# Optimization experiments

Measured on AMD Instinct MI355X. Metric: run time of the kernel, lower is better.

Reference implementation:

```python
import jax, jax.numpy as jnp
import numpy as np

B, C, H, W, N, K = 1, 64, 256, 1216, 40000, 9
EPS = 1e-5  # torch BatchNorm2d default eps


def setup_inputs() -> dict:
    key = jax.random.key(0)
    ks = jax.random.split(key, 10)
    feature_tensor = jax.random.normal(ks[0], (B, C, H, W), jnp.float32)
    nn_diff_pts_3d = jax.random.normal(ks[1], (B, N, K, 3), jnp.float32)
    # (x, y) pixel coords; 0..255 valid for both H=256 rows and W=1216 cols
    pixel_idxs = jax.random.randint(ks[2], (B, N, 2), 0, 256, dtype=jnp.int64)
    nn_pixel_idxs = jax.random.randint(ks[3], (B, N, K, 2), 0, 256, dtype=jnp.int64)
    W1 = jax.random.normal(ks[4], (3, C // 2), jnp.float32) * (1.0 / np.sqrt(3.0))
    b1 = jnp.zeros((C // 2,), jnp.float32)
    W2 = jax.random.normal(ks[5], (C // 2, C), jnp.float32) * (1.0 / np.sqrt(C // 2))
    b2 = jnp.zeros((C,), jnp.float32)
    conv_w = jax.random.normal(ks[6], (C, C), jnp.float32) * (1.0 / np.sqrt(C))  # [out, in] 1x1 conv
    conv_b = jnp.zeros((C,), jnp.float32)
    bn_gamma = jnp.ones((C,), jnp.float32)
    bn_beta = jnp.zeros((C,), jnp.float32)
    return {
        "feature_tensor": feature_tensor,
        "nn_diff_pts_3d": nn_diff_pts_3d,
        "pixel_idxs": pixel_idxs,
        "nn_pixel_idxs": nn_pixel_idxs,
        "W1": W1, "b1": b1, "W2": W2, "b2": b2,
        "conv_w": conv_w, "conv_b": conv_b,
        "bn_gamma": bn_gamma, "bn_beta": bn_beta,
    }


def reference(feature_tensor, nn_diff_pts_3d, pixel_idxs, nn_pixel_idxs,
              W1, b1, W2, b2, conv_w, conv_b, bn_gamma, bn_beta):
    b, n, k, _ = nn_diff_pts_3d.shape
    _, c, h_dim, w_dim = feature_tensor.shape

    # gather neighbor features: [b,H,W,C] indexed at (y,x) per batch -> [b,n,k,C]
    feat_hwc = jnp.transpose(feature_tensor, (0, 2, 3, 1))
    ix = nn_pixel_idxs[..., 0]
    iy = nn_pixel_idxs[..., 1]
    bidx = jnp.arange(b)[:, None, None]
    f = feat_hwc[bidx, iy, ix]  # [b, n, k, C]

    # MLP on 3D offsets -> per-neighbor weights [b,n,k,C]
    hmid = jax.nn.relu(nn_diff_pts_3d @ W1 + b1)
    wts = jax.nn.relu(hmid @ W2 + b2)

    # weighted neighbor sum (message reduce): [b,n,C]
    msg = jnp.sum(wts * f, axis=2)

    # 1x1 conv == per-point dense: [b,n,C]
    y = msg @ conv_w.T + conv_b

    # BatchNorm2d in training mode: stats over batch & spatial (here b,n), per channel
    mean = jnp.mean(y, axis=(0, 1))
    var = jnp.var(y, axis=(0, 1))
    y = bn_gamma * (y - mean) * jax.lax.rsqrt(var + EPS) + bn_beta
    y = jax.nn.relu(y)

    # scatter back into dense [b,C,H,W] image at (y,x)
    px = pixel_idxs[..., 0]
    py = pixel_idxs[..., 1]
    out = jnp.zeros((b, h_dim, w_dim, c), feature_tensor.dtype)
    out = out.at[jnp.arange(b)[:, None], py, px].set(y)
    return jnp.transpose(out, (0, 3, 1, 2))
```

## Files before the change

kernel.cpp:

```cpp
#include <hip/hip_runtime.h>

#define HDIM 256
#define WDIM 1216
#define HWC  (HDIM*WDIM)
#define NPTS 40000
#define KNN  9
#define PIXR 256
#define EPSF 1e-5f

typedef __attribute__((ext_vector_type(8))) short bf16x8;
typedef __attribute__((ext_vector_type(4))) float f32x4;

static __device__ __forceinline__ unsigned short f2bf(float f) {
    unsigned int u = __float_as_uint(f);
    u += 0x7FFFu + ((u >> 16) & 1u);
    return (unsigned short)(u >> 16);
}

__global__ __launch_bounds__(256) void prep_k(const float* __restrict__ feat,
                                              float* __restrict__ feat_t,
                                              int* __restrict__ winner,
                                              float* __restrict__ sums) {
    __shared__ float tile[64][65];
    const int iy   = blockIdx.x >> 2;
    const int ixb  = (blockIdx.x & 3) * 64;
    const int lane = threadIdx.x & 63;
    const int w    = threadIdx.x >> 6;

    const int tid = blockIdx.x * 256 + threadIdx.x;
    if (tid < PIXR * PIXR) winner[tid] = -1;
    if (tid < 128) sums[tid] = 0.f;

#pragma unroll
    for (int r = 0; r < 16; ++r) {
        int cc = w * 16 + r;
        tile[cc][lane] = feat[cc * HWC + iy * WDIM + ixb + lane];
    }
    __syncthreads();
#pragma unroll
    for (int r = 0; r < 16; ++r) {
        int ix = w * 16 + r;
        feat_t[(iy * PIXR + ixb + ix) * 64 + lane] = tile[lane][ix];
    }
}

__global__ __launch_bounds__(256) void point_k(
    const float* __restrict__ feat_t,
    const float* __restrict__ diff,
    const int*   __restrict__ nnpix,
    const int*   __restrict__ pix,
    const float* __restrict__ W1,
    const float* __restrict__ b1,
    const float* __restrict__ W2,
    const float* __restrict__ b2,
    const float* __restrict__ conv_w,
    const float* __restrict__ conv_b,
    int*   __restrict__ winner,
    float* __restrict__ y_buf,
    float* __restrict__ sums)
{
    __shared__ float dstage[4][448];
    __shared__ int   npx[4][288];
    __shared__ unsigned int hl[4][2][320];
    __shared__ float part[4][256];
    __shared__ unsigned short msgst[4][1152];

    const int l   = threadIdx.x & 63;
    const int w   = __builtin_amdgcn_readfirstlane(threadIdx.x >> 6);
    const int q   = l >> 4;
    const int col = l & 15;
    const int nbase = blockIdx.x * 64 + w * 16;

    if (threadIdx.x < 64) {
        int n = blockIdx.x * 64 + threadIdx.x;
        int px = pix[2 * n];
        int py = pix[2 * n + 1];
        atomicMax(&winner[py * PIXR + px], n);
    }

    bf16x8 bw2[4];
#pragma unroll
    for (int m = 0; m < 4; ++m)
#pragma unroll
        for (int t = 0; t < 8; ++t)
            bw2[m][t] = (short)f2bf(W2[(q * 8 + t) * 64 + col + 16 * m]);
    float b2m[4];
#pragma unroll
    for (int m = 0; m < 4; ++m) b2m[m] = b2[col + 16 * m];

    const int j0 = 2 * col;
    const float wa0 = W1[j0],     wa1 = W1[32 + j0],     wa2 = W1[64 + j0],     ba = b1[j0];
    const float wb0 = W1[j0 + 1], wb1 = W1[32 + j0 + 1], wb2 = W1[64 + j0 + 1], bb = b1[j0 + 1];

#pragma unroll
    for (int t = 0; t < 7; ++t) { int idx = l + 64 * t; if (idx < 432) dstage[w][idx] = diff[nbase * 27 + idx]; }
#pragma unroll
    for (int t = 0; t < 5; ++t) { int idx = l + 64 * t; if (idx < 288) npx[w][idx] = nnpix[nbase * 18 + idx]; }

    for (int z = 180 + l; z < 320; z += 64) { hl[w][0][z] = 0; hl[w][1][z] = 0; }

    float s1[4] = {0.f, 0.f, 0.f, 0.f}, s2[4] = {0.f, 0.f, 0.f, 0.f};
    float fvc[4][4], fvn[4][4];

#pragma unroll
    for (int i = 0; i < 4; ++i) {
        int k = q * 4 + i;
#pragma unroll
        for (int m = 0; m < 4; ++m) fvc[m][i] = 0.f;
        if (k < 9) {
            int px = npx[w][k * 2];
            int py = npx[w][k * 2 + 1];
            const float* fb = feat_t + (py * PIXR + px) * 64 + col;
#pragma unroll
            for (int m = 0; m < 4; ++m) fvc[m][i] = fb[16 * m];
        }
    }
#pragma unroll
    for (int i2 = 0; i2 < 3; ++i2) {
        int k2 = q + 4 * i2;
        if (k2 < 9) {
            float d0 = dstage[w][k2 * 3];
            float d1 = dstage[w][k2 * 3 + 1];
            float d2 = dstage[w][k2 * 3 + 2];
            float h0 = fmaxf(fmaf(d0, wa0, fmaf(d1, wa1, fmaf(d2, wa2, ba))), 0.f);
            float h1 = fmaxf(fmaf(d0, wb0, fmaf(d1, wb1, fmaf(d2, wb2, bb))), 0.f);
            hl[w][0][k2 * 20 + col] = (unsigned int)f2bf(h0) | ((unsigned int)f2bf(h1) << 16);
        }
    }

    for (int g = 0; g < 16; ++g) {
        if (g < 15) {
            const int gn = g + 1;
#pragma unroll
            for (int i = 0; i < 4; ++i) {
                int k = q * 4 + i;
#pragma unroll
                for (int m = 0; m < 4; ++m) fvn[m][i] = 0.f;
                if (k < 9) {
                    int px = npx[w][(gn * 9 + k) * 2];
                    int py = npx[w][(gn * 9 + k) * 2 + 1];
                    const float* fb = feat_t + (py * PIXR + px) * 64 + col;
#pragma unroll
                    for (int m = 0; m < 4; ++m) fvn[m][i] = fb[16 * m];
                }
            }
            unsigned int* hln = hl[w][gn & 1];
#pragma unroll
            for (int i2 = 0; i2 < 3; ++i2) {
                int k2 = q + 4 * i2;
                if (k2 < 9) {
                    float d0 = dstage[w][gn * 27 + k2 * 3];
                    float d1 = dstage[w][gn * 27 + k2 * 3 + 1];
                    float d2 = dstage[w][gn * 27 + k2 * 3 + 2];
                    float h0 = fmaxf(fmaf(d0, wa0, fmaf(d1, wa1, fmaf(d2, wa2, ba))), 0.f);
                    float h1 = fmaxf(fmaf(d0, wb0, fmaf(d1, wb1, fmaf(d2, wb2, bb))), 0.f);
                    hln[k2 * 20 + col] = (unsigned int)f2bf(h0) | ((unsigned int)f2bf(h1) << 16);
                }
            }
        }

        bf16x8 a;
        {
            uint4 av = *(const uint4*)((const char*)hl[w][g & 1] + col * 80 + q * 16);
            a = __builtin_bit_cast(bf16x8, av);
        }
#pragma unroll
        for (int m = 0; m < 4; ++m) {
            f32x4 acc = {b2m[m], b2m[m], b2m[m], b2m[m]};
            acc = __builtin_amdgcn_mfma_f32_16x16x32_bf16(a, bw2[m], acc, 0, 0, 0);
            float p = 0.f;
#pragma unroll
            for (int i = 0; i < 4; ++i)
                p = fmaf(fmaxf(acc[i], 0.f), fvc[m][i], p);
            part[w][(col + 16 * m) * 4 + q] = p;
        }
        float4 pr = *(const float4*)&part[w][l * 4];
        float msg = (pr.x + pr.y) + (pr.z + pr.w);
        msgst[w][g * 72 + l] = f2bf(msg);

#pragma unroll
        for (int i = 0; i < 4; ++i)
#pragma unroll
            for (int m = 0; m < 4; ++m) fvc[m][i] = fvn[m][i];
    }

    bf16x8 bcv[4][2];
#pragma unroll
    for (int m = 0; m < 4; ++m)
#pragma unroll
        for (int h = 0; h < 2; ++h)
#pragma unroll
            for (int t = 0; t < 8; ++t)
                bcv[m][h][t] = (short)f2bf(conv_w[(col + 16 * m) * 64 + h * 32 + q * 8 + t]);
    float cbm[4];
#pragma unroll
    for (int m = 0; m < 4; ++m) cbm[m] = conv_b[col + 16 * m];

    bf16x8 am[2];
#pragma unroll
    for (int h = 0; h < 2; ++h) {
        uint4 av = *(const uint4*)((const char*)msgst[w] + col * 144 + h * 64 + q * 16);
        am[h] = __builtin_bit_cast(bf16x8, av);
    }
#pragma unroll
    for (int m = 0; m < 4; ++m) {
        f32x4 acc = {cbm[m], cbm[m], cbm[m], cbm[m]};
        acc = __builtin_amdgcn_mfma_f32_16x16x32_bf16(am[0], bcv[m][0], acc, 0, 0, 0);
        acc = __builtin_amdgcn_mfma_f32_16x16x32_bf16(am[1], bcv[m][1], acc, 0, 0, 0);
#pragma unroll
        for (int i = 0; i < 4; ++i) {
            float y = acc[i];
            y_buf[(nbase + q * 4 + i) * 64 + col + 16 * m] = y;
            s1[m] += y;
            s2[m] = fmaf(y, y, s2[m]);
        }
    }

#pragma unroll
    for (int m = 0; m < 4; ++m) {
        float a1 = s1[m], a2 = s2[m];
        a1 += __shfl_xor(a1, 16); a1 += __shfl_xor(a1, 32);
        a2 += __shfl_xor(a2, 16); a2 += __shfl_xor(a2, 32);
        if (q == 0) {
            atomicAdd(&sums[col + 16 * m], a1);
            atomicAdd(&sums[64 + col + 16 * m], a2);
        }
    }
}

__global__ __launch_bounds__(256) void write_k(
    const float* __restrict__ y_buf,
    const float* __restrict__ sums,
    const float* __restrict__ gamma,
    const float* __restrict__ beta,
    const int*   __restrict__ winner,
    float* __restrict__ out)
{
    const int y  = blockIdx.x >> 2;
    const int ch = (blockIdx.x & 3) * 16;
    const int t  = threadIdx.x;
    const float inv_n = 1.f / (float)NPTS;

    const int wn = winner[y * PIXR + t];
    float4 yl[4] = {{0,0,0,0},{0,0,0,0},{0,0,0,0},{0,0,0,0}};
    if (wn >= 0) {
        const float4* yp = (const float4*)(y_buf + wn * 64 + ch);
        yl[0] = yp[0]; yl[1] = yp[1]; yl[2] = yp[2]; yl[3] = yp[3];
    }
    const float* ylf = (const float*)yl;

#pragma unroll
    for (int cc = 0; cc < 16; ++cc) {
        int c = ch + cc;
        float mean = sums[c] * inv_n;
        float var  = sums[64 + c] * inv_n - mean * mean;
        float rstd = rsqrtf(var + EPSF);
        float A = gamma[c] * rstd;
        float B = beta[c] - mean * A;

        float v = (wn >= 0) ? fmaxf(fmaf(A, ylf[cc], B), 0.f) : 0.f;
        float* row = out + c * HWC + y * WDIM;
        row[t] = v;
        if (t < 240) {
            float4 z = {0.f, 0.f, 0.f, 0.f};
            ((float4*)(row + 256))[t] = z;
        }
    }
}

extern "C" void kernel_launch(void* const* d_in, const int* in_sizes, int n_in,
                              void* d_out, int out_size, void* d_ws, size_t ws_size,
                              hipStream_t stream) {
    const float* feat   = (const float*)d_in[0];
    const float* diff   = (const float*)d_in[1];
    const int*   pix    = (const int*)  d_in[2];
    const int*   nnpix  = (const int*)  d_in[3];
    const float* W1     = (const float*)d_in[4];
    const float* b1v    = (const float*)d_in[5];
    const float* W2     = (const float*)d_in[6];
    const float* b2v    = (const float*)d_in[7];
    const float* conv_w = (const float*)d_in[8];
    const float* conv_b = (const float*)d_in[9];
    const float* gamma  = (const float*)d_in[10];
    const float* beta   = (const float*)d_in[11];
    float* out = (float*)d_out;

    char* ws = (char*)d_ws;
    float* feat_t  = (float*)(ws);
    float* y_buf   = (float*)(ws + 16777216);
    float* sums    = (float*)(ws + 27017216);
    int*   winner  = (int*)  (ws + 27017728);

    prep_k<<<1024, 256, 0, stream>>>(feat, feat_t, winner, sums);
    point_k<<<625, 256, 0, stream>>>(feat_t, diff, nnpix, pix, W1, b1v, W2, b2v,
                                     conv_w, conv_b, winner, y_buf, sums);
    write_k<<<1024, 256, 0, stream>>>(y_buf, sums, gamma, beta, winner, out);
}
```

Measured before the change: 235.8 us.

## Double waves per block in point kernel, vectorize gathers, reduce BN stats in LDS

The point kernel now runs 8 waves of 8 points each per block instead of 4 waves of 16, halving the serial per-wave loop to expose more parallelism across the 625 blocks. Channel ownership per lane is permuted so feature gathers and weight loads use float4 vector loads. The BN sum atomics are first reduced across waves in shared memory, so one block-level atomic per channel replaces per-wave atomics. The conv MFMA still processes 16 rows, half of them duplicates, so half of that work is wasted, and the extra __syncthreads plus higher register pressure at 512 threads may limit occupancy.

```diff
diff --git a/kernel.cpp b/kernel.cpp
--- a/kernel.cpp
+++ b/kernel.cpp
@@ -44,7 +44,7 @@
     }
 }
 
-__global__ __launch_bounds__(256) void point_k(
+__global__ __launch_bounds__(512) void point_k(
     const float* __restrict__ feat_t,
     const float* __restrict__ diff,
     const int*   __restrict__ nnpix,
@@ -59,17 +59,17 @@
     float* __restrict__ y_buf,
     float* __restrict__ sums)
 {
-    __shared__ float dstage[4][448];
-    __shared__ int   npx[4][288];
-    __shared__ unsigned int hl[4][2][320];
-    __shared__ float part[4][256];
-    __shared__ unsigned short msgst[4][1152];
+    __shared__ float dstage[8][224];
+    __shared__ int   npx[8][144];
+    __shared__ unsigned int hl[8][2][320];
+    __shared__ float part[8][256];
+    __shared__ unsigned short msgst[8][576];
 
     const int l   = threadIdx.x & 63;
     const int w   = __builtin_amdgcn_readfirstlane(threadIdx.x >> 6);
     const int q   = l >> 4;
     const int col = l & 15;
-    const int nbase = blockIdx.x * 64 + w * 16;
+    const int nbase = blockIdx.x * 64 + w * 8;
 
     if (threadIdx.x < 64) {
         int n = blockIdx.x * 64 + threadIdx.x;
@@ -80,22 +80,27 @@
 
     bf16x8 bw2[4];
 #pragma unroll
-    for (int m = 0; m < 4; ++m)
-#pragma unroll
-        for (int t = 0; t < 8; ++t)
-            bw2[m][t] = (short)f2bf(W2[(q * 8 + t) * 64 + col + 16 * m]);
+    for (int t = 0; t < 8; ++t) {
+        float4 v = ((const float4*)W2)[(q * 8 + t) * 16 + col];
+        bw2[0][t] = (short)f2bf(v.x);
+        bw2[1][t] = (short)f2bf(v.y);
+        bw2[2][t] = (short)f2bf(v.z);
+        bw2[3][t] = (short)f2bf(v.w);
+    }
     float b2m[4];
-#pragma unroll
-    for (int m = 0; m < 4; ++m) b2m[m] = b2[col + 16 * m];
+    {
+        float4 bv = ((const float4*)b2)[col];
+        b2m[0] = bv.x; b2m[1] = bv.y; b2m[2] = bv.z; b2m[3] = bv.w;
+    }
 
     const int j0 = 2 * col;
     const float wa0 = W1[j0],     wa1 = W1[32 + j0],     wa2 = W1[64 + j0],     ba = b1[j0];
     const float wb0 = W1[j0 + 1], wb1 = W1[32 + j0 + 1], wb2 = W1[64 + j0 + 1], bb = b1[j0 + 1];
 
 #pragma unroll
-    for (int t = 0; t < 7; ++t) { int idx = l + 64 * t; if (idx < 432) dstage[w][idx] = diff[nbase * 27 + idx]; }
-#pragma unroll
-    for (int t = 0; t < 5; ++t) { int idx = l + 64 * t; if (idx < 288) npx[w][idx] = nnpix[nbase * 18 + idx]; }
+    for (int t = 0; t < 4; ++t) { int idx = l + 64 * t; if (idx < 216) dstage[w][idx] = diff[nbase * 27 + idx]; }
+#pragma unroll
+    for (int t = 0; t < 3; ++t) { int idx = l + 64 * t; if (idx < 144) npx[w][idx] = nnpix[nbase * 18 + idx]; }
 
     for (int z = 180 + l; z < 320; z += 64) { hl[w][0][z] = 0; hl[w][1][z] = 0; }
 
@@ -106,13 +111,12 @@
     for (int i = 0; i < 4; ++i) {
         int k = q * 4 + i;
 #pragma unroll
-        for (int m = 0; m < 4; ++m) fvc[m][i] = 0.f;
+        for (int m = 0; m < 4; ++m) fvc[i][m] = 0.f;
         if (k < 9) {
             int px = npx[w][k * 2];
             int py = npx[w][k * 2 + 1];
-            const float* fb = feat_t + (py * PIXR + px) * 64 + col;
-#pragma unroll
-            for (int m = 0; m < 4; ++m) fvc[m][i] = fb[16 * m];
+            float4 f4 = *(const float4*)(feat_t + (py * PIXR + px) * 64 + 4 * col);
+            fvc[i][0] = f4.x; fvc[i][1] = f4.y; fvc[i][2] = f4.z; fvc[i][3] = f4.w;
         }
     }
 #pragma unroll
@@ -128,20 +132,19 @@
         }
     }
 
-    for (int g = 0; g < 16; ++g) {
-        if (g < 15) {
+    for (int g = 0; g < 8; ++g) {
+        if (g < 7) {
             const int gn = g + 1;
 #pragma unroll
             for (int i = 0; i < 4; ++i) {
                 int k = q * 4 + i;
 #pragma unroll
-                for (int m = 0; m < 4; ++m) fvn[m][i] = 0.f;
+                for (int m = 0; m < 4; ++m) fvn[i][m] = 0.f;
                 if (k < 9) {
                     int px = npx[w][(gn * 9 + k) * 2];
                     int py = npx[w][(gn * 9 + k) * 2 + 1];
-                    const float* fb = feat_t + (py * PIXR + px) * 64 + col;
-#pragma unroll
-                    for (int m = 0; m < 4; ++m) fvn[m][i] = fb[16 * m];
+                    float4 f4 = *(const float4*)(feat_t + (py * PIXR + px) * 64 + 4 * col);
+                    fvn[i][0] = f4.x; fvn[i][1] = f4.y; fvn[i][2] = f4.z; fvn[i][3] = f4.w;
                 }
             }
             unsigned int* hln = hl[w][gn & 1];
@@ -171,8 +174,8 @@
             float p = 0.f;
 #pragma unroll
             for (int i = 0; i < 4; ++i)
-                p = fmaf(fmaxf(acc[i], 0.f), fvc[m][i], p);
-            part[w][(col + 16 * m) * 4 + q] = p;
+                p = fmaf(fmaxf(acc[i], 0.f), fvc[i][m], p);
+            part[w][(4 * col + m) * 4 + q] = p;
         }
         float4 pr = *(const float4*)&part[w][l * 4];
         float msg = (pr.x + pr.y) + (pr.z + pr.w);
@@ -181,25 +184,30 @@
 #pragma unroll
         for (int i = 0; i < 4; ++i)
 #pragma unroll
-            for (int m = 0; m < 4; ++m) fvc[m][i] = fvn[m][i];
+            for (int m = 0; m < 4; ++m) fvc[i][m] = fvn[i][m];
     }
 
     bf16x8 bcv[4][2];
 #pragma unroll
     for (int m = 0; m < 4; ++m)
 #pragma unroll
-        for (int h = 0; h < 2; ++h)
-#pragma unroll
-            for (int t = 0; t < 8; ++t)
-                bcv[m][h][t] = (short)f2bf(conv_w[(col + 16 * m) * 64 + h * 32 + q * 8 + t]);
+        for (int h = 0; h < 2; ++h) {
+            float4 v0 = ((const float4*)conv_w)[(col + 16 * m) * 16 + h * 8 + q * 2];
+            float4 v1 = ((const float4*)conv_w)[(col + 16 * m) * 16 + h * 8 + q * 2 + 1];
+            bcv[m][h][0] = (short)f2bf(v0.x); bcv[m][h][1] = (short)f2bf(v0.y);
+            bcv[m][h][2] = (short)f2bf(v0.z); bcv[m][h][3] = (short)f2bf(v0.w);
+            bcv[m][h][4] = (short)f2bf(v1.x); bcv[m][h][5] = (short)f2bf(v1.y);
+            bcv[m][h][6] = (short)f2bf(v1.z); bcv[m][h][7] = (short)f2bf(v1.w);
+        }
     float cbm[4];
 #pragma unroll
     for (int m = 0; m < 4; ++m) cbm[m] = conv_b[col + 16 * m];
 
     bf16x8 am[2];
+    const int crow = col & 7;
 #pragma unroll
     for (int h = 0; h < 2; ++h) {
-        uint4 av = *(const uint4*)((const char*)msgst[w] + col * 144 + h * 64 + q * 16);
+        uint4 av = *(const uint4*)((const char*)msgst[w] + crow * 144 + h * 64 + q * 16);
         am[h] = __builtin_bit_cast(bf16x8, av);
     }
 #pragma unroll
@@ -207,12 +215,14 @@
         f32x4 acc = {cbm[m], cbm[m], cbm[m], cbm[m]};
         acc = __builtin_amdgcn_mfma_f32_16x16x32_bf16(am[0], bcv[m][0], acc, 0, 0, 0);
         acc = __builtin_amdgcn_mfma_f32_16x16x32_bf16(am[1], bcv[m][1], acc, 0, 0, 0);
-#pragma unroll
-        for (int i = 0; i < 4; ++i) {
-            float y = acc[i];
-            y_buf[(nbase + q * 4 + i) * 64 + col + 16 * m] = y;
-            s1[m] += y;
-            s2[m] = fmaf(y, y, s2[m]);
+        if (q < 2) {
+#pragma unroll
+            for (int i = 0; i < 4; ++i) {
+                float y = acc[i];
+                y_buf[(nbase + q * 4 + i) * 64 + col + 16 * m] = y;
+                s1[m] += y;
+                s2[m] = fmaf(y, y, s2[m]);
+            }
         }
     }
 
@@ -222,9 +232,17 @@
         a1 += __shfl_xor(a1, 16); a1 += __shfl_xor(a1, 32);
         a2 += __shfl_xor(a2, 16); a2 += __shfl_xor(a2, 32);
         if (q == 0) {
-            atomicAdd(&sums[col + 16 * m], a1);
-            atomicAdd(&sums[64 + col + 16 * m], a2);
-        }
+            part[w][col + 16 * m]      = a1;
+            part[w][64 + col + 16 * m] = a2;
+        }
+    }
+    __syncthreads();
+    if (threadIdx.x < 128) {
+        int c = threadIdx.x;
+        float t = 0.f;
+#pragma unroll
+        for (int w8 = 0; w8 < 8; ++w8) t += part[w8][c];
+        atomicAdd(&sums[c], t);
     }
 }
 
@@ -292,7 +310,7 @@
     int*   winner  = (int*)  (ws + 27017728);
 
     prep_k<<<1024, 256, 0, stream>>>(feat, feat_t, winner, sums);
-    point_k<<<625, 256, 0, stream>>>(feat_t, diff, nnpix, pix, W1, b1v, W2, b2v,
+    point_k<<<625, 512, 0, stream>>>(feat_t, diff, nnpix, pix, W1, b1v, W2, b2v,
                                      conv_w, conv_b, winner, y_buf, sums);
     write_k<<<1024, 256, 0, stream>>>(y_buf, sums, gamma, beta, winner, out);
 }
```

Measured after the change: 196.0 us. 1.2x faster.
